# Optimization experiments

Measured on AMD Instinct MI355X. Metric: run time of the kernel, lower is better.

The kernel has to match this reference:

```python
import jax, jax.numpy as jnp
import numpy as np
from jax import lax

B, C, H, W = 8, 256, 128, 128
RED = 16


def _disk(r):
    yy, xx = np.mgrid[-r:r + 1, -r:r + 1]
    return ((xx * xx + yy * yy) <= r * r).astype(np.float32)


def _se_conv(m, se):
    kern = jnp.asarray(se)[None, None]  # [1,1,k,k]
    return lax.conv_general_dilated(m, kern, (1, 1), 'SAME',
                                    dimension_numbers=('NCHW', 'OIHW', 'NCHW'))


def _dilate(m, se):
    return (_se_conv(m, se) > 0.5).astype(m.dtype)


def _erode(m, se):
    return (_se_conv(m, se) > float(se.sum()) - 0.5).astype(m.dtype)


def _morph(mask):
    # GPU-friendly analogue of morphologic_process (skimage CPU round-trip):
    # invert, opening(disk2) ~ remove_small_objects(20), closing(disk1) ~
    # remove_small_holes(10), pad-3 binary_closing(disk3), crop, invert.
    d1, d2, d3 = _disk(1), _disk(2), _disk(3)
    m = 1.0 - mask
    m = _dilate(_erode(m, d2), d2)
    m = _erode(_dilate(m, d1), d1)
    mp = jnp.pad(m, ((0, 0), (0, 0), (3, 3), (3, 3)))
    mp = _erode(_dilate(mp, d3), d3)
    return 1.0 - mp[:, :, 3:-3, 3:-3]


def _conv1x1(x, w, b):
    return jnp.einsum('oi,bihw->bohw', w, x) + b[None, :, None, None]


def _avg3(x):
    # torch AvgPool2d(3,1,1) with count_include_pad=True -> always /9
    return lax.reduce_window(x, 0.0, lax.add, (1, 1, 3, 3), (1, 1, 1, 1), 'SAME') / 9.0


def _max3(x):
    return lax.reduce_window(x, -jnp.inf, lax.max, (1, 1, 3, 3), (1, 1, 1, 1), 'SAME')


def setup_inputs() -> dict:
    key = jax.random.key(0)
    ks = iter(jax.random.split(key, 32))
    s = 0.05
    d = {
        'x_p': jax.random.normal(next(ks), (B, C, H, W), jnp.float32),
        'x_c': jax.random.normal(next(ks), (B, C, H, W), jnp.float32),
        # PALayer: conv_p (shared two 1x1), conv_c (2c->c)
        'pa_w1': jax.random.normal(next(ks), (C, C), jnp.float32) * s,
        'pa_b1': jnp.zeros((C,), jnp.float32),
        'pa_w2': jax.random.normal(next(ks), (C, C), jnp.float32) * s,
        'pa_b2': jnp.zeros((C,), jnp.float32),
        'pa_wc': jax.random.normal(next(ks), (C, 2 * C), jnp.float32) * s,
        'pa_bc': jnp.zeros((C,), jnp.float32),
        # CALayer: conv_avg and conv_max (c -> c/16 -> c)
        'ca_aw1': jax.random.normal(next(ks), (C // RED, C), jnp.float32) * s,
        'ca_ab1': jnp.zeros((C // RED,), jnp.float32),
        'ca_aw2': jax.random.normal(next(ks), (C, C // RED), jnp.float32) * s,
        'ca_ab2': jnp.zeros((C,), jnp.float32),
        'ca_mw1': jax.random.normal(next(ks), (C // RED, C), jnp.float32) * s,
        'ca_mb1': jnp.zeros((C // RED,), jnp.float32),
        'ca_mw2': jax.random.normal(next(ks), (C, C // RED), jnp.float32) * s,
        'ca_mb2': jnp.zeros((C,), jnp.float32),
        # b1/b2/b3 1x1 convs
        'b1_w': jax.random.normal(next(ks), (C, C), jnp.float32) * s,
        'b1_b': jnp.zeros((C,), jnp.float32),
        'b2_w': jax.random.normal(next(ks), (C, C), jnp.float32) * s,
        'b2_b': jnp.zeros((C,), jnp.float32),
        'b3_w': jax.random.normal(next(ks), (C, C), jnp.float32) * s,
        'b3_b': jnp.zeros((C,), jnp.float32),
        # fusion: (2c+1) -> c
        'fus_w': jax.random.normal(next(ks), (C, 2 * C + 1), jnp.float32) * s,
        'fus_b': jnp.zeros((C,), jnp.float32),
    }
    return d


def reference(x_p, x_c, pa_w1, pa_b1, pa_w2, pa_b2, pa_wc, pa_bc,
              ca_aw1, ca_ab1, ca_aw2, ca_ab2, ca_mw1, ca_mb1, ca_mw2, ca_mb2,
              b1_w, b1_b, b2_w, b2_b, b3_w, b3_b, fus_w, fus_b):
    b, c, h, w = x_p.shape
    # --- PALayer(x_p) ---
    y1 = _avg3(x_p)
    y2 = _max3(x_p)
    y3 = _conv1x1(jax.nn.relu(_conv1x1(y1, pa_w1, pa_b1)), pa_w2, pa_b2)
    y4 = _conv1x1(jax.nn.relu(_conv1x1(y2, pa_w1, pa_b1)), pa_w2, pa_b2)
    pa_gate = jax.nn.sigmoid(_conv1x1(jnp.concatenate([y1 + y3, y2 + y4], axis=1), pa_wc, pa_bc))
    buffer_p = pa_gate * x_p
    # --- CALayer(x_c) ---
    a = jnp.mean(x_c, axis=(2, 3), keepdims=True)
    m = jnp.max(x_c, axis=(2, 3), keepdims=True)
    ya = _conv1x1(jax.nn.relu(_conv1x1(a, ca_aw1, ca_ab1)), ca_aw2, ca_ab2)
    ym = _conv1x1(jax.nn.relu(_conv1x1(m, ca_mw1, ca_mb1)), ca_mw2, ca_mb2)
    buffer_c = jax.nn.sigmoid(ya + ym) * x_c
    # --- cross-modal width attention ---
    Q1 = _conv1x1(buffer_p, b1_w, b1_b)
    S1 = _conv1x1(buffer_c, b2_w, b2_b)
    M_c_to_p = jax.nn.softmax(jnp.einsum('bchi,bchj->bhij', Q1, S1), axis=-1)
    Q2 = _conv1x1(buffer_c, b1_w, b1_b)
    S2 = _conv1x1(buffer_p, b2_w, b2_b)
    M_p_to_c = jax.nn.softmax(jnp.einsum('bchi,bchj->bhij', Q2, S2), axis=-1)
    # validity mask (detached) + morphology
    V = (jnp.sum(lax.stop_gradient(M_p_to_c), axis=2) > 0.1).astype(x_p.dtype)  # [b,h,w]
    V = _morph(V[:, None])  # [b,1,h,w]
    # attend b3(x_c) with M_c_to_p
    v3 = _conv1x1(x_c, b3_w, b3_b)
    buf = jnp.einsum('bhij,bchj->bchi', M_c_to_p, v3)
    out = _conv1x1(jnp.concatenate([buf, x_p, V], axis=1), fus_w, fus_b)
    return out
```

## Files before the change

### kernel.cpp

```cpp
#include <hip/hip_runtime.h>
#include <hip/hip_bf16.h>
#include <math.h>

#define BB 8
#define CC 256
#define HH 128
#define WW 128
#define HWSZ (HH*WW)
#define NTOT ((size_t)BB*CC*HWSZ)

typedef __hip_bfloat16 bf16;
typedef __attribute__((ext_vector_type(8))) short short8v;
typedef __attribute__((ext_vector_type(4))) float f32x4;

__device__ __forceinline__ float ldf(const float* p) { return *p; }
__device__ __forceinline__ float ldf(const bf16* p) { return __bfloat162float(*p); }
__device__ __forceinline__ void stf(float* p, float v) { *p = v; }
__device__ __forceinline__ void stf(bf16* p, float v) { *p = __float2bfloat16(v); }

union bfu { bf16 b; unsigned short u; };
__device__ __forceinline__ unsigned short f2bf_bits(float v) { bfu c; c.b = __float2bfloat16(v); return c.u; }
__device__ __forceinline__ float bfbits2f(unsigned short u) { bfu c; c.u = u; return __bfloat162float(c.b); }
__device__ __forceinline__ unsigned pk2(float a, float b) {
    return (unsigned)f2bf_bits(a) | ((unsigned)f2bf_bits(b) << 16);
}

__global__ __launch_bounds__(256) void pool3_kernel(const float* __restrict__ x,
                                                    bf16* __restrict__ yavg,
                                                    bf16* __restrict__ ymax) {
    size_t idx = (size_t)blockIdx.x * 256 + threadIdx.x;
    int w0 = (int)(idx & 15) * 8;
    int h = (int)(idx >> 4) & 127;
    size_t bc = idx >> 11;
    const float* base = x + bc * HWSZ;
    float ts[8], tm[8];
#pragma unroll
    for (int i = 0; i < 8; ++i) { ts[i] = 0.f; tm[i] = -INFINITY; }
#pragma unroll
    for (int dy = -1; dy <= 1; ++dy) {
        int hh = h + dy;
        if (hh < 0 || hh >= HH) continue;
        const float* rp = base + hh * WW + w0;
        float4 v0 = *(const float4*)rp;
        float4 v1 = *(const float4*)(rp + 4);
        float s9[10], m9[10];
        s9[1] = v0.x; s9[2] = v0.y; s9[3] = v0.z; s9[4] = v0.w;
        s9[5] = v1.x; s9[6] = v1.y; s9[7] = v1.z; s9[8] = v1.w;
#pragma unroll
        for (int i = 1; i < 9; ++i) m9[i] = s9[i];
        if (w0 > 0)      { float L = rp[-1]; s9[0] = L; m9[0] = L; }
        else             { s9[0] = 0.f; m9[0] = -INFINITY; }
        if (w0 < WW - 8) { float R = rp[8]; s9[9] = R; m9[9] = R; }
        else             { s9[9] = 0.f; m9[9] = -INFINITY; }
#pragma unroll
        for (int i = 0; i < 8; ++i) {
            ts[i] += s9[i] + s9[i + 1] + s9[i + 2];
            tm[i] = fmaxf(tm[i], fmaxf(m9[i], fmaxf(m9[i + 1], m9[i + 2])));
        }
    }
    uint4 ua, um;
    ua.x = pk2(ts[0] * (1.f/9.f), ts[1] * (1.f/9.f));
    ua.y = pk2(ts[2] * (1.f/9.f), ts[3] * (1.f/9.f));
    ua.z = pk2(ts[4] * (1.f/9.f), ts[5] * (1.f/9.f));
    ua.w = pk2(ts[6] * (1.f/9.f), ts[7] * (1.f/9.f));
    um.x = pk2(tm[0], tm[1]); um.y = pk2(tm[2], tm[3]);
    um.z = pk2(tm[4], tm[5]); um.w = pk2(tm[6], tm[7]);
    *(uint4*)(yavg + idx * 8) = ua;
    *(uint4*)(ymax + idx * 8) = um;
}

#define EPI_NONE   0
#define EPI_RELU   1
#define EPI_ADDAUX 2
#define EPI_SIGMUL 3

#define BMP 128
#define BNO 128
#define BKC 64
#define LDK 72

template<bool SC, class T>
__device__ __forceinline__ unsigned short ld_bits(const T* p, float s);
template<> __device__ __forceinline__ unsigned short ld_bits<false, bf16>(const bf16* p, float) {
    bfu c; c.b = *p; return c.u;
}
template<> __device__ __forceinline__ unsigned short ld_bits<true, bf16>(const bf16* p, float s) {
    return f2bf_bits(__bfloat162float(*p) * s);
}
template<> __device__ __forceinline__ unsigned short ld_bits<false, float>(const float* p, float) {
    return f2bf_bits(*p);
}
template<> __device__ __forceinline__ unsigned short ld_bits<true, float>(const float* p, float s) {
    return f2bf_bits(*p * s);
}

template<bool SC, class T>
__device__ __forceinline__ void stage_X(short* __restrict__ Xs,
                                        const T* __restrict__ in,
                                        const float* __restrict__ scale,
                                        int b, int cbase, size_t pbase, int tid)
{
    const int xp  = tid & 127;
    const int xkh = (tid >> 7) * 32;
    const T* src = in + ((size_t)b * 256 + cbase + xkh) * HWSZ + pbase + xp;
    short* dst = Xs + xp * LDK + xkh;
#pragma unroll
    for (int ch = 0; ch < 2; ++ch) {
        unsigned short us[16];
#pragma unroll
        for (int g = 0; g < 4; ++g) {
#pragma unroll
            for (int r = 0; r < 4; ++r) {
                int kloc = ch * 16 + g * 4 + r;
                float sc = SC ? scale[b * 256 + cbase + xkh + kloc] : 1.f;
                us[g * 4 + r] = ld_bits<SC, T>(src + (size_t)kloc * HWSZ, sc);
            }
        }
#pragma unroll
        for (int g = 0; g < 4; ++g) {
            uint2 wv;
            wv.x = (unsigned)us[g * 4 + 0] | ((unsigned)us[g * 4 + 1] << 16);
            wv.y = (unsigned)us[g * 4 + 2] | ((unsigned)us[g * 4 + 3] << 16);
            *(uint2*)(dst + g * 8 + ch * 4) = wv;
        }
    }
}

__device__ __forceinline__ void stage_W(short* __restrict__ Wh, short* __restrict__ Wl,
                                        const float* __restrict__ Wm, int WS,
                                        int obase, int k0, int tid)
{
    const int wo  = tid >> 1;
    const int wkh = (tid & 1) * 32;
    const float* wrow = Wm + (size_t)(obase + wo) * WS + k0 + wkh;
    short* dh = Wh + wo * LDK + wkh;
    short* dl = Wl + wo * LDK + wkh;
#pragma unroll
    for (int ch = 0; ch < 2; ++ch) {
        unsigned short uh[16], ul[16];
#pragma unroll
        for (int g = 0; g < 4; ++g) {
#pragma unroll
            for (int r = 0; r < 4; ++r) {
                float v = wrow[ch * 16 + g * 4 + r];
                unsigned short hb = f2bf_bits(v);
                uh[g * 4 + r] = hb;
                ul[g * 4 + r] = f2bf_bits(v - bfbits2f(hb));
            }
        }
#pragma unroll
        for (int g = 0; g < 4; ++g) {
            uint2 a, c;
            a.x = (unsigned)uh[g*4+0] | ((unsigned)uh[g*4+1] << 16);
            a.y = (unsigned)uh[g*4+2] | ((unsigned)uh[g*4+3] << 16);
            c.x = (unsigned)ul[g*4+0] | ((unsigned)ul[g*4+1] << 16);
            c.y = (unsigned)ul[g*4+2] | ((unsigned)ul[g*4+3] << 16);
            *(uint2*)(dh + g * 8 + ch * 4) = a;
            *(uint2*)(dl + g * 8 + ch * 4) = c;
        }
    }
}

__device__ __forceinline__ void stage_rm(short* __restrict__ Xs, const bf16* __restrict__ src,
                                         size_t rstride, int k0, int tid)
{
    const int row = tid & 127;
    const int kh = (tid >> 7) * 32;
    const short* sp = (const short*)src + (size_t)row * rstride + k0 + kh;
    short* dst = Xs + row * LDK + kh;
#pragma unroll
    for (int q = 0; q < 4; ++q) {
        short8v v = *(const short8v*)(sp + q * 8);
        uint2 lo, hi;
        lo.x = (unsigned)(unsigned short)v[0] | ((unsigned)(unsigned short)v[1] << 16);
        lo.y = (unsigned)(unsigned short)v[2] | ((unsigned)(unsigned short)v[3] << 16);
        hi.x = (unsigned)(unsigned short)v[4] | ((unsigned)(unsigned short)v[5] << 16);
        hi.y = (unsigned)(unsigned short)v[6] | ((unsigned)(unsigned short)v[7] << 16);
        *(uint2*)(dst + ((2*q) & 3) * 8 + (q >> 1) * 4) = lo;
        *(uint2*)(dst + ((2*q+1) & 3) * 8 + (q >> 1) * 4) = hi;
    }
}

__device__ __forceinline__ void load4f(const bf16* p, float* v) {
    ushort4 u = *(const ushort4*)p;
    v[0] = bfbits2f(u.x); v[1] = bfbits2f(u.y); v[2] = bfbits2f(u.z); v[3] = bfbits2f(u.w);
}
__device__ __forceinline__ void load4f(const float* p, float* v) {
    float4 u = *(const float4*)p;
    v[0] = u.x; v[1] = u.y; v[2] = u.z; v[3] = u.w;
}
__device__ __forceinline__ void store4(bf16* p, const float* v) {
    uint2 u;
    u.x = pk2(v[0], v[1]);
    u.y = pk2(v[2], v[3]);
    *(uint2*)p = u;
}
__device__ __forceinline__ void store4(float* p, const float* v) {
    *(float4*)p = make_float4(v[0], v[1], v[2], v[3]);
}

template<int MODE, bool TWO_IN, bool HAS_SCALE, bool HAS_V,
         class TIN1, class TIN2, class TAUX, class TOUT>
__global__ __launch_bounds__(256) void conv1x1_kernel(
    TOUT* __restrict__ out,
    const TIN1* __restrict__ in1,
    const TIN2* __restrict__ in2,
    const float* __restrict__ Wm, int WS,
    const float* __restrict__ bias,
    const TAUX* __restrict__ aux,
    const float* __restrict__ scale,
    const float* __restrict__ vvec,
    const float* __restrict__ vw)
{
    const int K = TWO_IN ? 512 : 256;
    __shared__ __align__(16) short Xs[BMP * LDK];
    __shared__ __align__(16) short Wh[BNO * LDK];
    __shared__ __align__(16) short Wl[BNO * LDK];
    const int tid = threadIdx.x;
    const int b = blockIdx.z;
    const size_t p0 = (size_t)blockIdx.x * BMP;
    const int o0 = blockIdx.y * BNO;
    const int lane = tid & 63, wave = tid >> 6;
    const int wr = wave >> 1, wc = wave & 1;
    const int lrow = lane & 15, lg = lane >> 4;

    f32x4 acc[4][4];
#pragma unroll
    for (int mi = 0; mi < 4; ++mi)
#pragma unroll
        for (int ni = 0; ni < 4; ++ni) acc[mi][ni] = (f32x4)(0.f);

    for (int kt = 0; kt < K / BKC; ++kt) {
        const int k0 = kt * BKC;
        stage_W(Wh, Wl, Wm, WS, o0, k0, tid);
        if (TWO_IN && k0 >= 256)
            stage_X<false, TIN2>(Xs, in2, nullptr, b, k0 - 256, p0, tid);
        else
            stage_X<HAS_SCALE, TIN1>(Xs, in1, scale, b, k0, p0, tid);
        __syncthreads();
#pragma unroll
        for (int kk = 0; kk < 2; ++kk) {
            short8v af[4], bh[4], bl[4];
#pragma unroll
            for (int mi = 0; mi < 4; ++mi)
                af[mi] = *(const short8v*)&Xs[(wr * 64 + mi * 16 + lrow) * LDK + kk * 32 + lg * 8];
#pragma unroll
            for (int ni = 0; ni < 4; ++ni) {
                bh[ni] = *(const short8v*)&Wh[(wc * 64 + ni * 16 + lrow) * LDK + kk * 32 + lg * 8];
                bl[ni] = *(const short8v*)&Wl[(wc * 64 + ni * 16 + lrow) * LDK + kk * 32 + lg * 8];
            }
#pragma unroll
            for (int mi = 0; mi < 4; ++mi)
#pragma unroll
                for (int ni = 0; ni < 4; ++ni)
                    acc[mi][ni] = __builtin_amdgcn_mfma_f32_16x16x32_bf16(af[mi], bh[ni], acc[mi][ni], 0, 0, 0);
#pragma unroll
            for (int mi = 0; mi < 4; ++mi)
#pragma unroll
                for (int ni = 0; ni < 4; ++ni)
                    acc[mi][ni] = __builtin_amdgcn_mfma_f32_16x16x32_bf16(af[mi], bl[ni], acc[mi][ni], 0, 0, 0);
        }
        __syncthreads();
    }

#pragma unroll
    for (int ni = 0; ni < 4; ++ni) {
        const int o = o0 + wc * 64 + ni * 16 + lrow;
        const float bs = bias[o];
        const float vwo = HAS_V ? vw[(size_t)o * WS] : 0.f;
#pragma unroll
        for (int mi = 0; mi < 4; ++mi) {
            const size_t p = p0 + wr * 64 + mi * 16 + lg * 4;
            const size_t oidx = ((size_t)b * CC + o) * HWSZ + p;
            float auxv[4];
            if (MODE == EPI_ADDAUX || MODE == EPI_SIGMUL) load4f(&aux[oidx], auxv);
            float vv[4];
            if (HAS_V) load4f(&vvec[(size_t)b * HWSZ + p], vv);
            float vals[4];
#pragma unroll
            for (int r = 0; r < 4; ++r) {
                float val = acc[mi][ni][r] + bs;
                if (HAS_V) val += vwo * vv[r];
                if (MODE == EPI_RELU)        val = fmaxf(val, 0.f);
                else if (MODE == EPI_ADDAUX) val += auxv[r];
                else if (MODE == EPI_SIGMUL) val = (1.f / (1.f + __expf(-val))) * auxv[r];
                vals[r] = val;
            }
            store4(&out[oidx], vals);
        }
    }
}

__global__ __launch_bounds__(256) void ca_reduce_kernel(const float* __restrict__ xc,
                                                        float* __restrict__ avgv,
                                                        float* __restrict__ maxv) {
    int bc = blockIdx.x;
    const float4* base = (const float4*)(xc + (size_t)bc * HWSZ);
    float s = 0.f, mx = -INFINITY;
    for (int i = threadIdx.x; i < HWSZ / 4; i += 256) {
        float4 v = base[i];
        s += v.x + v.y + v.z + v.w;
        mx = fmaxf(mx, fmaxf(fmaxf(v.x, v.y), fmaxf(v.z, v.w)));
    }
    for (int off = 32; off; off >>= 1) {
        s += __shfl_down(s, off);
        mx = fmaxf(mx, __shfl_down(mx, off));
    }
    __shared__ float ss[4], sm[4];
    int wid = threadIdx.x >> 6, lane = threadIdx.x & 63;
    if (lane == 0) { ss[wid] = s; sm[wid] = mx; }
    __syncthreads();
    if (threadIdx.x == 0) {
        float S = ss[0] + ss[1] + ss[2] + ss[3];
        float M = fmaxf(fmaxf(sm[0], sm[1]), fmaxf(sm[2], sm[3]));
        avgv[bc] = S * (1.f / HWSZ);
        maxv[bc] = M;
    }
}

__global__ __launch_bounds__(256) void ca_mlp_kernel(
    const float* __restrict__ avgv, const float* __restrict__ maxv,
    const float* __restrict__ aw1, const float* __restrict__ ab1,
    const float* __restrict__ aw2, const float* __restrict__ ab2,
    const float* __restrict__ mw1, const float* __restrict__ mb1,
    const float* __restrict__ mw2, const float* __restrict__ mb2,
    float* __restrict__ gate) {
    int b = blockIdx.x;
    __shared__ float av[256], mv[256], ha[16], hm[16];
    int t = threadIdx.x;
    av[t] = avgv[b * 256 + t];
    mv[t] = maxv[b * 256 + t];
    __syncthreads();
    if (t < 16) {
        float s = ab1[t];
        for (int i = 0; i < 256; ++i) s += aw1[t * 256 + i] * av[i];
        ha[t] = fmaxf(s, 0.f);
    } else if (t < 32) {
        int r = t - 16;
        float s = mb1[r];
        for (int i = 0; i < 256; ++i) s += mw1[r * 256 + i] * mv[i];
        hm[r] = fmaxf(s, 0.f);
    }
    __syncthreads();
    float ya = ab2[t], ym = mb2[t];
    for (int r = 0; r < 16; ++r) {
        ya += aw2[t * 16 + r] * ha[r];
        ym += mw2[t * 16 + r] * hm[r];
    }
    float g = ya + ym;
    gate[b * 256 + t] = 1.f / (1.f + __expf(-g));
}

template<bool STORE_M>
__global__ __launch_bounds__(256) void attn_kernel(
    const bf16* __restrict__ Q, const bf16* __restrict__ S,
    bf16* __restrict__ Mout, float* __restrict__ m0out)
{
    int bh = blockIdx.x; int b = bh >> 7, h = bh & 127;
    const bf16* Qb = Q + (size_t)b * CC * HWSZ + h * WW;
    const bf16* Sb = S + (size_t)b * CC * HWSZ + h * WW;
    __shared__ __align__(16) short Qs[128 * LDK];
    __shared__ __align__(16) short Ss[128 * LDK];
    const int tid = threadIdx.x;
    const int lane = tid & 63, wave = tid >> 6;
    const int lrow = lane & 15, lg = lane >> 4;

    f32x4 acc[2][8];
#pragma unroll
    for (int mi = 0; mi < 2; ++mi)
#pragma unroll
        for (int ni = 0; ni < 8; ++ni) acc[mi][ni] = (f32x4)(0.f);

    for (int kt = 0; kt < 4; ++kt) {
        const int k0 = kt * 64;
        {
            const int xp = tid & 127, xkh = (tid >> 7) * 32;
            const bf16* sq = Qb + (size_t)(k0 + xkh) * HWSZ + xp;
            const bf16* ssrc = Sb + (size_t)(k0 + xkh) * HWSZ + xp;
            short* dq = Qs + xp * LDK + xkh;
            short* ds = Ss + xp * LDK + xkh;
#pragma unroll
            for (int ch = 0; ch < 2; ++ch) {
#pragma unroll
                for (int g = 0; g < 4; ++g) {
                    unsigned short uq[4], us[4];
#pragma unroll
                    for (int r = 0; r < 4; ++r) {
                        int kloc = ch * 16 + g * 4 + r;
                        bfu cq; cq.b = sq[(size_t)kloc * HWSZ]; uq[r] = cq.u;
                        bfu cs2; cs2.b = ssrc[(size_t)kloc * HWSZ]; us[r] = cs2.u;
                    }
                    uint2 wq, ws;
                    wq.x = (unsigned)uq[0] | ((unsigned)uq[1] << 16);
                    wq.y = (unsigned)uq[2] | ((unsigned)uq[3] << 16);
                    ws.x = (unsigned)us[0] | ((unsigned)us[1] << 16);
                    ws.y = (unsigned)us[2] | ((unsigned)us[3] << 16);
                    *(uint2*)(dq + g * 8 + ch * 4) = wq;
                    *(uint2*)(ds + g * 8 + ch * 4) = ws;
                }
            }
        }
        __syncthreads();
#pragma unroll
        for (int kk = 0; kk < 2; ++kk) {
            short8v qa[2], sv[8];
#pragma unroll
            for (int mi = 0; mi < 2; ++mi)
                qa[mi] = *(const short8v*)&Qs[(wave * 32 + mi * 16 + lrow) * LDK + kk * 32 + lg * 8];
#pragma unroll
            for (int ni = 0; ni < 8; ++ni)
                sv[ni] = *(const short8v*)&Ss[(ni * 16 + lrow) * LDK + kk * 32 + lg * 8];
#pragma unroll
            for (int mi = 0; mi < 2; ++mi)
#pragma unroll
                for (int ni = 0; ni < 8; ++ni)
                    acc[mi][ni] = __builtin_amdgcn_mfma_f32_16x16x32_bf16(qa[mi], sv[ni], acc[mi][ni], 0, 0, 0);
        }
        __syncthreads();
    }

#pragma unroll
    for (int mi = 0; mi < 2; ++mi) {
#pragma unroll
        for (int r = 0; r < 4; ++r) {
            float mx = acc[mi][0][r];
#pragma unroll
            for (int ni = 1; ni < 8; ++ni) mx = fmaxf(mx, acc[mi][ni][r]);
            for (int m = 1; m < 16; m <<= 1) mx = fmaxf(mx, __shfl_xor(mx, m));
            float sm = 0.f;
#pragma unroll
            for (int ni = 0; ni < 8; ++ni) {
                float e = __expf(acc[mi][ni][r] - mx);
                acc[mi][ni][r] = e; sm += e;
            }
            for (int m = 1; m < 16; m <<= 1) sm += __shfl_xor(sm, m);
            float inv = 1.f / sm;
#pragma unroll
            for (int ni = 0; ni < 8; ++ni) acc[mi][ni][r] *= inv;
        }
    }

    if (STORE_M) {
        bf16* Mb = Mout + (size_t)bh * WW * WW;
#pragma unroll
        for (int mi = 0; mi < 2; ++mi)
#pragma unroll
            for (int r = 0; r < 4; ++r) {
                int i = wave * 32 + mi * 16 + lg * 4 + r;
#pragma unroll
                for (int ni = 0; ni < 8; ++ni)
                    stf(&Mb[i * WW + ni * 16 + lrow], acc[mi][ni][r]);
            }
    } else {
        __shared__ float cs[16][128];
#pragma unroll
        for (int ni = 0; ni < 8; ++ni) {
            float s = 0.f;
#pragma unroll
            for (int mi = 0; mi < 2; ++mi)
#pragma unroll
                for (int r = 0; r < 4; ++r) s += acc[mi][ni][r];
            cs[wave * 4 + lg][ni * 16 + lrow] = s;
        }
        __syncthreads();
        if (tid < 128) {
            float s = 0.f;
#pragma unroll
            for (int g = 0; g < 16; ++g) s += cs[g][tid];
            m0out[(size_t)b * HWSZ + h * WW + tid] = (s > 0.1f) ? 0.f : 1.f;
        }
    }
}

__global__ __launch_bounds__(256) void attn_apply_kernel(
    const bf16* __restrict__ Mbuf, const bf16* __restrict__ v3,
    bf16* __restrict__ outb)
{
    int bh = blockIdx.x; int b = bh >> 7, h = bh & 127;
    int ch0 = blockIdx.y * 128;
    const bf16* Mb = Mbuf + (size_t)bh * WW * WW;
    const bf16* Vb = v3 + ((size_t)b * CC + ch0) * HWSZ + h * WW;
    bf16* Ob = outb + ((size_t)b * CC + ch0) * HWSZ + h * WW;
    __shared__ __align__(16) short Ms[128 * LDK];
    __shared__ __align__(16) short Vs[128 * LDK];
    const int tid = threadIdx.x;
    const int lane = tid & 63, wave = tid >> 6;
    const int lrow = lane & 15, lg = lane >> 4;

    f32x4 acc[2][8];
#pragma unroll
    for (int mi = 0; mi < 2; ++mi)
#pragma unroll
        for (int ni = 0; ni < 8; ++ni) acc[mi][ni] = (f32x4)(0.f);

    for (int kt = 0; kt < 2; ++kt) {
        const int k0 = kt * 64;
        stage_rm(Ms, Mb, WW, k0, tid);
        stage_rm(Vs, Vb, HWSZ, k0, tid);
        __syncthreads();
#pragma unroll
        for (int kk = 0; kk < 2; ++kk) {
            short8v ma[2], vv[8];
#pragma unroll
            for (int mi = 0; mi < 2; ++mi)
                ma[mi] = *(const short8v*)&Ms[(wave * 32 + mi * 16 + lrow) * LDK + kk * 32 + lg * 8];
#pragma unroll
            for (int ni = 0; ni < 8; ++ni)
                vv[ni] = *(const short8v*)&Vs[(ni * 16 + lrow) * LDK + kk * 32 + lg * 8];
#pragma unroll
            for (int mi = 0; mi < 2; ++mi)
#pragma unroll
                for (int ni = 0; ni < 8; ++ni)
                    acc[mi][ni] = __builtin_amdgcn_mfma_f32_16x16x32_bf16(ma[mi], vv[ni], acc[mi][ni], 0, 0, 0);
        }
        __syncthreads();
    }

#pragma unroll
    for (int ni = 0; ni < 8; ++ni) {
        const int c = ni * 16 + lrow;
#pragma unroll
        for (int mi = 0; mi < 2; ++mi) {
            const int i0 = wave * 32 + mi * 16 + lg * 4;
            float vals[4] = { acc[mi][ni][0], acc[mi][ni][1], acc[mi][ni][2], acc[mi][ni][3] };
            store4(&Ob[(size_t)c * HWSZ + i0], vals);
        }
    }
}

__global__ void morph_kernel(const float* __restrict__ in, float* __restrict__ out,
                             int Hd, int Wd, int r, float thresh) {
    int idx = blockIdx.x * 256 + threadIdx.x;
    int tot = BB * Hd * Wd;
    if (idx >= tot) return;
    int x = idx % Wd; int y = (idx / Wd) % Hd; int b = idx / (Wd * Hd);
    const float* base = in + (size_t)b * Hd * Wd;
    float s = 0.f;
    for (int dy = -r; dy <= r; ++dy) {
        int yy = y + dy; if (yy < 0 || yy >= Hd) continue;
        for (int dx = -r; dx <= r; ++dx) {
            if (dx * dx + dy * dy > r * r) continue;
            int xx = x + dx; if (xx < 0 || xx >= Wd) continue;
            s += base[yy * Wd + xx];
        }
    }
    out[idx] = (s > thresh) ? 1.f : 0.f;
}

__global__ void pad3_kernel(const float* __restrict__ in, float* __restrict__ out) {
    int idx = blockIdx.x * 256 + threadIdx.x;
    int tot = BB * 134 * 134; if (idx >= tot) return;
    int x = idx % 134; int y = (idx / 134) % 134; int b = idx / (134 * 134);
    float v = 0.f;
    int xs = x - 3, ys = y - 3;
    if (xs >= 0 && xs < 128 && ys >= 0 && ys < 128)
        v = in[((size_t)b * 128 + ys) * 128 + xs];
    out[idx] = v;
}

__global__ void vfinal_kernel(const float* __restrict__ in, float* __restrict__ V) {
    int idx = blockIdx.x * 256 + threadIdx.x;
    if (idx >= BB * HWSZ) return;
    int x = idx & 127; int y = (idx >> 7) & 127; int b = idx >> 14;
    V[idx] = 1.f - in[((size_t)b * 134 + y + 3) * 134 + (x + 3)];
}

extern "C" void kernel_launch(void* const* d_in, const int* in_sizes, int n_in,
                              void* d_out, int out_size, void* d_ws, size_t ws_size,
                              hipStream_t stream) {
    const float* x_p   = (const float*)d_in[0];
    const float* x_c   = (const float*)d_in[1];
    const float* pa_w1 = (const float*)d_in[2];
    const float* pa_b1 = (const float*)d_in[3];
    const float* pa_w2 = (const float*)d_in[4];
    const float* pa_b2 = (const float*)d_in[5];
    const float* pa_wc = (const float*)d_in[6];
    const float* pa_bc = (const float*)d_in[7];
    const float* ca_aw1 = (const float*)d_in[8];
    const float* ca_ab1 = (const float*)d_in[9];
    const float* ca_aw2 = (const float*)d_in[10];
    const float* ca_ab2 = (const float*)d_in[11];
    const float* ca_mw1 = (const float*)d_in[12];
    const float* ca_mb1 = (const float*)d_in[13];
    const float* ca_mw2 = (const float*)d_in[14];
    const float* ca_mb2 = (const float*)d_in[15];
    const float* b1_w  = (const float*)d_in[16];
    const float* b1_b  = (const float*)d_in[17];
    const float* b2_w  = (const float*)d_in[18];
    const float* b2_b  = (const float*)d_in[19];
    const float* b3_w  = (const float*)d_in[20];
    const float* b3_b  = (const float*)d_in[21];
    const float* fus_w = (const float*)d_in[22];
    const float* fus_b = (const float*)d_in[23];
    float* out = (float*)d_out;

    char* wsb = (char*)d_ws;
    bf16* A  = (bf16*)wsb;
    bf16* Bb = (bf16*)(wsb + NTOT * 2);
    float* smalls = (float*)(wsb + NTOT * 4);
    float* avgv = smalls;
    float* maxv = smalls + 2048;
    float* gate = smalls + 4096;
    float* mph0 = smalls + 6144;
    float* mph1 = mph0 + 143648;
    float* Vfin = mph1 + 143648;
    bf16* D1 = (bf16*)d_out;
    bf16* D2 = D1 + NTOT;
    bf16* Mbuf = D1;

    dim3 cgrid(HWSZ / BMP, CC / BNO, BB);
    const int TPB = 256;

    pool3_kernel<<<NTOT / 8 / 256, TPB, 0, stream>>>(x_p, A, Bb);
    conv1x1_kernel<EPI_RELU, false, false, false, bf16, bf16, bf16, bf16>
        <<<cgrid, TPB, 0, stream>>>(D1, A, nullptr, pa_w1, 256, pa_b1,
                                    nullptr, nullptr, nullptr, nullptr);
    conv1x1_kernel<EPI_ADDAUX, false, false, false, bf16, bf16, bf16, bf16>
        <<<cgrid, TPB, 0, stream>>>(D2, D1, nullptr, pa_w2, 256, pa_b2,
                                    A, nullptr, nullptr, nullptr);
    conv1x1_kernel<EPI_RELU, false, false, false, bf16, bf16, bf16, bf16>
        <<<cgrid, TPB, 0, stream>>>(A, Bb, nullptr, pa_w1, 256, pa_b1,
                                    nullptr, nullptr, nullptr, nullptr);
    conv1x1_kernel<EPI_ADDAUX, false, false, false, bf16, bf16, bf16, bf16>
        <<<cgrid, TPB, 0, stream>>>(D1, A, nullptr, pa_w2, 256, pa_b2,
                                    Bb, nullptr, nullptr, nullptr);
    conv1x1_kernel<EPI_SIGMUL, true, false, false, bf16, bf16, float, bf16>
        <<<cgrid, TPB, 0, stream>>>(A, D2, D1, pa_wc, 512, pa_bc,
                                    x_p, nullptr, nullptr, nullptr);

    ca_reduce_kernel<<<BB * CC, TPB, 0, stream>>>(x_c, avgv, maxv);
    ca_mlp_kernel<<<BB, TPB, 0, stream>>>(avgv, maxv, ca_aw1, ca_ab1, ca_aw2, ca_ab2,
                                          ca_mw1, ca_mb1, ca_mw2, ca_mb2, gate);

    conv1x1_kernel<EPI_NONE, false, false, false, bf16, bf16, bf16, bf16>
        <<<cgrid, TPB, 0, stream>>>(Bb, A, nullptr, b1_w, 256, b1_b,
                                    nullptr, nullptr, nullptr, nullptr);
    conv1x1_kernel<EPI_NONE, false, false, false, bf16, bf16, bf16, bf16>
        <<<cgrid, TPB, 0, stream>>>(D1, A, nullptr, b2_w, 256, b2_b,
                                    nullptr, nullptr, nullptr, nullptr);
    conv1x1_kernel<EPI_NONE, false, true, false, float, float, float, bf16>
        <<<cgrid, TPB, 0, stream>>>(A, x_c, nullptr, b1_w, 256, b1_b,
                                    nullptr, gate, nullptr, nullptr);
    conv1x1_kernel<EPI_NONE, false, true, false, float, float, float, bf16>
        <<<cgrid, TPB, 0, stream>>>(D2, x_c, nullptr, b2_w, 256, b2_b,
                                    nullptr, gate, nullptr, nullptr);

    attn_kernel<false><<<BB * HH, TPB, 0, stream>>>(A, D1, nullptr, mph0);
    attn_kernel<true><<<BB * HH, TPB, 0, stream>>>(Bb, D2, Mbuf, nullptr);

    conv1x1_kernel<EPI_NONE, false, false, false, float, float, float, bf16>
        <<<cgrid, TPB, 0, stream>>>(A, x_c, nullptr, b3_w, 256, b3_b,
                                    nullptr, nullptr, nullptr, nullptr);

    morph_kernel<<<512, TPB, 0, stream>>>(mph0, mph1, 128, 128, 2, 12.5f);
    morph_kernel<<<512, TPB, 0, stream>>>(mph1, mph0, 128, 128, 2, 0.5f);
    morph_kernel<<<512, TPB, 0, stream>>>(mph0, mph1, 128, 128, 1, 0.5f);
    morph_kernel<<<512, TPB, 0, stream>>>(mph1, mph0, 128, 128, 1, 4.5f);
    pad3_kernel<<<562, TPB, 0, stream>>>(mph0, mph1);
    morph_kernel<<<562, TPB, 0, stream>>>(mph1, mph0, 134, 134, 3, 0.5f);
    morph_kernel<<<562, TPB, 0, stream>>>(mph0, mph1, 134, 134, 3, 28.5f);
    vfinal_kernel<<<512, TPB, 0, stream>>>(mph1, Vfin);

    attn_apply_kernel<<<dim3(BB * HH, 2), TPB, 0, stream>>>(Mbuf, A, Bb);
    conv1x1_kernel<EPI_NONE, true, false, true, bf16, float, float, float>
        <<<cgrid, TPB, 0, stream>>>(out, Bb, x_p, fus_w, 513, fus_b,
                                    nullptr, nullptr, Vfin, fus_w + 512);
}
```

Baseline: 1.563 ms.

## Pre-split weights into swizzled bf16 tiles and load via global_load_lds

```diff
diff --git a/kernel.cpp b/kernel.cpp
--- a/kernel.cpp
+++ b/kernel.cpp
@@ -23,6 +23,12 @@
 __device__ __forceinline__ float bfbits2f(unsigned short u) { bfu c; c.u = u; return __bfloat162float(c.b); }
 __device__ __forceinline__ unsigned pk2(float a, float b) {
     return (unsigned)f2bf_bits(a) | ((unsigned)f2bf_bits(b) << 16);
+}
+
+__device__ __forceinline__ void gld16(const void* g, void* l) {
+    __builtin_amdgcn_global_load_lds(
+        (const __attribute__((address_space(1))) unsigned int*)(uintptr_t)g,
+        (__attribute__((address_space(3))) unsigned int*)(uintptr_t)l, 16, 0, 0);
 }
 
 __global__ __launch_bounds__(256) void pool3_kernel(const float* __restrict__ x,
@@ -69,6 +75,33 @@
     *(uint4*)(ymax + idx * 8) = um;
 }
 
+__global__ __launch_bounds__(256) void prep_w_kernel(
+    const float* __restrict__ w0, const float* __restrict__ w1,
+    const float* __restrict__ w2, const float* __restrict__ w3,
+    const float* __restrict__ w4, const float* __restrict__ w5,
+    const float* __restrict__ w6, short* __restrict__ dst)
+{
+    int gid = blockIdx.x * 256 + threadIdx.x;
+    const float* src; int K, WS, local; size_t dofs;
+    if (gid < 65536)       { src = w0; K = 256; WS = 256; dofs = 0;      local = gid; }
+    else if (gid < 131072) { src = w1; K = 256; WS = 256; dofs = 131072; local = gid - 65536; }
+    else if (gid < 262144) { src = w2; K = 512; WS = 512; dofs = 262144; local = gid - 131072; }
+    else if (gid < 327680) { src = w3; K = 256; WS = 256; dofs = 524288; local = gid - 262144; }
+    else if (gid < 393216) { src = w4; K = 256; WS = 256; dofs = 655360; local = gid - 327680; }
+    else if (gid < 458752) { src = w5; K = 256; WS = 256; dofs = 786432; local = gid - 393216; }
+    else                   { src = w6; K = 512; WS = 513; dofs = 917504; local = gid - 458752; }
+    int o = (K == 256) ? (local >> 8) : (local >> 9);
+    int k = local & (K - 1);
+    int kt = k >> 6, k6 = k & 63, k5 = k6 & 31;
+    int pos = (k6 >> 5) * 32 + ((k5 >> 2) & 3) * 8 + (k5 >> 4) * 4 + (k5 & 3);
+    pos ^= (o & 7) << 3;
+    size_t off = dofs + (size_t)(o >> 7) * K * 128 + (size_t)kt * 8192 + (size_t)(o & 127) * 64 + pos;
+    float v = src[(size_t)o * WS + k];
+    unsigned short hb = f2bf_bits(v);
+    dst[off] = (short)hb;
+    dst[off + (size_t)256 * K] = (short)f2bf_bits(v - bfbits2f(hb));
+}
+
 #define EPI_NONE   0
 #define EPI_RELU   1
 #define EPI_ADDAUX 2
@@ -76,8 +109,6 @@
 
 #define BMP 128
 #define BNO 128
-#define BKC 64
-#define LDK 72
 
 template<bool SC, class T>
 __device__ __forceinline__ unsigned short ld_bits(const T* p, float s);
@@ -103,61 +134,23 @@
     const int xp  = tid & 127;
     const int xkh = (tid >> 7) * 32;
     const T* src = in + ((size_t)b * 256 + cbase + xkh) * HWSZ + pbase + xp;
-    short* dst = Xs + xp * LDK + xkh;
-#pragma unroll
-    for (int ch = 0; ch < 2; ++ch) {
-        unsigned short us[16];
-#pragma unroll
-        for (int g = 0; g < 4; ++g) {
-#pragma unroll
-            for (int r = 0; r < 4; ++r) {
-                int kloc = ch * 16 + g * 4 + r;
-                float sc = SC ? scale[b * 256 + cbase + xkh + kloc] : 1.f;
-                us[g * 4 + r] = ld_bits<SC, T>(src + (size_t)kloc * HWSZ, sc);
-            }
-        }
-#pragma unroll
-        for (int g = 0; g < 4; ++g) {
-            uint2 wv;
-            wv.x = (unsigned)us[g * 4 + 0] | ((unsigned)us[g * 4 + 1] << 16);
-            wv.y = (unsigned)us[g * 4 + 2] | ((unsigned)us[g * 4 + 3] << 16);
-            *(uint2*)(dst + g * 8 + ch * 4) = wv;
-        }
-    }
-}
-
-__device__ __forceinline__ void stage_W(short* __restrict__ Wh, short* __restrict__ Wl,
-                                        const float* __restrict__ Wm, int WS,
-                                        int obase, int k0, int tid)
-{
-    const int wo  = tid >> 1;
-    const int wkh = (tid & 1) * 32;
-    const float* wrow = Wm + (size_t)(obase + wo) * WS + k0 + wkh;
-    short* dh = Wh + wo * LDK + wkh;
-    short* dl = Wl + wo * LDK + wkh;
-#pragma unroll
-    for (int ch = 0; ch < 2; ++ch) {
-        unsigned short uh[16], ul[16];
-#pragma unroll
-        for (int g = 0; g < 4; ++g) {
-#pragma unroll
-            for (int r = 0; r < 4; ++r) {
-                float v = wrow[ch * 16 + g * 4 + r];
-                unsigned short hb = f2bf_bits(v);
-                uh[g * 4 + r] = hb;
-                ul[g * 4 + r] = f2bf_bits(v - bfbits2f(hb));
-            }
-        }
-#pragma unroll
-        for (int g = 0; g < 4; ++g) {
-            uint2 a, c;
-            a.x = (unsigned)uh[g*4+0] | ((unsigned)uh[g*4+1] << 16);
-            a.y = (unsigned)uh[g*4+2] | ((unsigned)uh[g*4+3] << 16);
-            c.x = (unsigned)ul[g*4+0] | ((unsigned)ul[g*4+1] << 16);
-            c.y = (unsigned)ul[g*4+2] | ((unsigned)ul[g*4+3] << 16);
-            *(uint2*)(dh + g * 8 + ch * 4) = a;
-            *(uint2*)(dl + g * 8 + ch * 4) = c;
-        }
+    const float* scp = SC ? (scale + b * 256 + cbase + xkh) : nullptr;
+    const int swz = (xp & 7) << 3;
+    short* dst = Xs + xp * 64;
+#pragma unroll
+    for (int g = 0; g < 4; ++g) {
+        unsigned short u[8];
+#pragma unroll
+        for (int j = 0; j < 8; ++j) {
+            int k5 = (j >> 2) * 16 + g * 4 + (j & 3);
+            u[j] = ld_bits<SC, T>(src + (size_t)k5 * HWSZ, SC ? scp[k5] : 1.f);
+        }
+        uint4 wv;
+        wv.x = (unsigned)u[0] | ((unsigned)u[1] << 16);
+        wv.y = (unsigned)u[2] | ((unsigned)u[3] << 16);
+        wv.z = (unsigned)u[4] | ((unsigned)u[5] << 16);
+        wv.w = (unsigned)u[6] | ((unsigned)u[7] << 16);
+        *(uint4*)(dst + ((xkh + g * 8) ^ swz)) = wv;
     }
 }
 
@@ -167,17 +160,25 @@
     const int row = tid & 127;
     const int kh = (tid >> 7) * 32;
     const short* sp = (const short*)src + (size_t)row * rstride + k0 + kh;
-    short* dst = Xs + row * LDK + kh;
-#pragma unroll
-    for (int q = 0; q < 4; ++q) {
-        short8v v = *(const short8v*)(sp + q * 8);
-        uint2 lo, hi;
-        lo.x = (unsigned)(unsigned short)v[0] | ((unsigned)(unsigned short)v[1] << 16);
-        lo.y = (unsigned)(unsigned short)v[2] | ((unsigned)(unsigned short)v[3] << 16);
-        hi.x = (unsigned)(unsigned short)v[4] | ((unsigned)(unsigned short)v[5] << 16);
-        hi.y = (unsigned)(unsigned short)v[6] | ((unsigned)(unsigned short)v[7] << 16);
-        *(uint2*)(dst + ((2*q) & 3) * 8 + (q >> 1) * 4) = lo;
-        *(uint2*)(dst + ((2*q+1) & 3) * 8 + (q >> 1) * 4) = hi;
+    const int swz = (row & 7) << 3;
+    short* dst = Xs + row * 64;
+    short8v lv[4];
+#pragma unroll
+    for (int q = 0; q < 4; ++q) lv[q] = *(const short8v*)(sp + q * 8);
+#pragma unroll
+    for (int g = 0; g < 4; ++g) {
+        unsigned short u[8];
+#pragma unroll
+        for (int r = 0; r < 4; ++r) {
+            u[r]     = (unsigned short)lv[g >> 1][(g & 1) * 4 + r];
+            u[4 + r] = (unsigned short)lv[2 + (g >> 1)][(g & 1) * 4 + r];
+        }
+        uint4 wv;
+        wv.x = (unsigned)u[0] | ((unsigned)u[1] << 16);
+        wv.y = (unsigned)u[2] | ((unsigned)u[3] << 16);
+        wv.z = (unsigned)u[4] | ((unsigned)u[5] << 16);
+        wv.w = (unsigned)u[6] | ((unsigned)u[7] << 16);
+        *(uint4*)(dst + ((kh + g * 8) ^ swz)) = wv;
     }
 }
 
@@ -205,24 +206,26 @@
     TOUT* __restrict__ out,
     const TIN1* __restrict__ in1,
     const TIN2* __restrict__ in2,
-    const float* __restrict__ Wm, int WS,
+    const short* __restrict__ Wp,
     const float* __restrict__ bias,
     const TAUX* __restrict__ aux,
     const float* __restrict__ scale,
     const float* __restrict__ vvec,
-    const float* __restrict__ vw)
+    const float* __restrict__ vw, int vws)
 {
     const int K = TWO_IN ? 512 : 256;
-    __shared__ __align__(16) short Xs[BMP * LDK];
-    __shared__ __align__(16) short Wh[BNO * LDK];
-    __shared__ __align__(16) short Wl[BNO * LDK];
+    __shared__ __align__(16) short Xs[BMP * 64];
+    __shared__ __align__(16) short Wh[BNO * 64];
+    __shared__ __align__(16) short Wl[BNO * 64];
     const int tid = threadIdx.x;
     const int b = blockIdx.z;
     const size_t p0 = (size_t)blockIdx.x * BMP;
     const int o0 = blockIdx.y * BNO;
-    const int lane = tid & 63, wave = tid >> 6;
+    const int lane = tid & 63;
+    const int wave = tid >> 6;
     const int wr = wave >> 1, wc = wave & 1;
     const int lrow = lane & 15, lg = lane >> 4;
+    const int sA = (lrow & 7) << 3;
 
     f32x4 acc[4][4];
 #pragma unroll
@@ -230,9 +233,19 @@
 #pragma unroll
         for (int ni = 0; ni < 4; ++ni) acc[mi][ni] = (f32x4)(0.f);
 
-    for (int kt = 0; kt < K / BKC; ++kt) {
-        const int k0 = kt * BKC;
-        stage_W(Wh, Wl, Wm, WS, o0, k0, tid);
+    for (int kt = 0; kt < K / 64; ++kt) {
+        const int k0 = kt * 64;
+        {
+            const short* gWh = Wp + (size_t)(o0 >> 7) * K * 128 + (size_t)kt * 8192;
+            const short* gWl = gWh + (size_t)256 * K;
+            const int wofs = wave * 4096;
+            const int lb = lane * 16;
+#pragma unroll
+            for (int q = 0; q < 4; ++q) {
+                gld16((const char*)gWh + wofs + q * 1024 + lb, (char*)Wh + wofs + q * 1024);
+                gld16((const char*)gWl + wofs + q * 1024 + lb, (char*)Wl + wofs + q * 1024);
+            }
+        }
         if (TWO_IN && k0 >= 256)
             stage_X<false, TIN2>(Xs, in2, nullptr, b, k0 - 256, p0, tid);
         else
@@ -240,14 +253,15 @@
         __syncthreads();
 #pragma unroll
         for (int kk = 0; kk < 2; ++kk) {
+            const int kofs = kk * 32 + lg * 8;
             short8v af[4], bh[4], bl[4];
 #pragma unroll
             for (int mi = 0; mi < 4; ++mi)
-                af[mi] = *(const short8v*)&Xs[(wr * 64 + mi * 16 + lrow) * LDK + kk * 32 + lg * 8];
+                af[mi] = *(const short8v*)&Xs[(wr * 64 + mi * 16 + lrow) * 64 + (kofs ^ sA)];
 #pragma unroll
             for (int ni = 0; ni < 4; ++ni) {
-                bh[ni] = *(const short8v*)&Wh[(wc * 64 + ni * 16 + lrow) * LDK + kk * 32 + lg * 8];
-                bl[ni] = *(const short8v*)&Wl[(wc * 64 + ni * 16 + lrow) * LDK + kk * 32 + lg * 8];
+                bh[ni] = *(const short8v*)&Wh[(wc * 64 + ni * 16 + lrow) * 64 + (kofs ^ sA)];
+                bl[ni] = *(const short8v*)&Wl[(wc * 64 + ni * 16 + lrow) * 64 + (kofs ^ sA)];
             }
 #pragma unroll
             for (int mi = 0; mi < 4; ++mi)
@@ -267,7 +281,7 @@
     for (int ni = 0; ni < 4; ++ni) {
         const int o = o0 + wc * 64 + ni * 16 + lrow;
         const float bs = bias[o];
-        const float vwo = HAS_V ? vw[(size_t)o * WS] : 0.f;
+        const float vwo = HAS_V ? vw[(size_t)o * vws] : 0.f;
 #pragma unroll
         for (int mi = 0; mi < 4; ++mi) {
             const size_t p = p0 + wr * 64 + mi * 16 + lg * 4;
@@ -359,11 +373,12 @@
     int bh = blockIdx.x; int b = bh >> 7, h = bh & 127;
     const bf16* Qb = Q + (size_t)b * CC * HWSZ + h * WW;
     const bf16* Sb = S + (size_t)b * CC * HWSZ + h * WW;
-    __shared__ __align__(16) short Qs[128 * LDK];
-    __shared__ __align__(16) short Ss[128 * LDK];
+    __shared__ __align__(16) short Qs[128 * 64];
+    __shared__ __align__(16) short Ss[128 * 64];
     const int tid = threadIdx.x;
     const int lane = tid & 63, wave = tid >> 6;
     const int lrow = lane & 15, lg = lane >> 4;
+    const int sA = (lrow & 7) << 3;
 
     f32x4 acc[2][8];
 #pragma unroll
@@ -377,39 +392,42 @@
             const int xp = tid & 127, xkh = (tid >> 7) * 32;
             const bf16* sq = Qb + (size_t)(k0 + xkh) * HWSZ + xp;
             const bf16* ssrc = Sb + (size_t)(k0 + xkh) * HWSZ + xp;
-            short* dq = Qs + xp * LDK + xkh;
-            short* ds = Ss + xp * LDK + xkh;
-#pragma unroll
-            for (int ch = 0; ch < 2; ++ch) {
-#pragma unroll
-                for (int g = 0; g < 4; ++g) {
-                    unsigned short uq[4], us[4];
-#pragma unroll
-                    for (int r = 0; r < 4; ++r) {
-                        int kloc = ch * 16 + g * 4 + r;
-                        bfu cq; cq.b = sq[(size_t)kloc * HWSZ]; uq[r] = cq.u;
-                        bfu cs2; cs2.b = ssrc[(size_t)kloc * HWSZ]; us[r] = cs2.u;
-                    }
-                    uint2 wq, ws;
-                    wq.x = (unsigned)uq[0] | ((unsigned)uq[1] << 16);
-                    wq.y = (unsigned)uq[2] | ((unsigned)uq[3] << 16);
-                    ws.x = (unsigned)us[0] | ((unsigned)us[1] << 16);
-                    ws.y = (unsigned)us[2] | ((unsigned)us[3] << 16);
-                    *(uint2*)(dq + g * 8 + ch * 4) = wq;
-                    *(uint2*)(ds + g * 8 + ch * 4) = ws;
+            const int swz = (xp & 7) << 3;
+            short* dq = Qs + xp * 64;
+            short* dsx = Ss + xp * 64;
+#pragma unroll
+            for (int g = 0; g < 4; ++g) {
+                unsigned short uq[8], us[8];
+#pragma unroll
+                for (int j = 0; j < 8; ++j) {
+                    int k5 = (j >> 2) * 16 + g * 4 + (j & 3);
+                    bfu cq; cq.b = sq[(size_t)k5 * HWSZ]; uq[j] = cq.u;
+                    bfu cs2; cs2.b = ssrc[(size_t)k5 * HWSZ]; us[j] = cs2.u;
                 }
+                uint4 a, s2;
+                a.x = (unsigned)uq[0] | ((unsigned)uq[1] << 16);
+                a.y = (unsigned)uq[2] | ((unsigned)uq[3] << 16);
+                a.z = (unsigned)uq[4] | ((unsigned)uq[5] << 16);
+                a.w = (unsigned)uq[6] | ((unsigned)uq[7] << 16);
+                s2.x = (unsigned)us[0] | ((unsigned)us[1] << 16);
+                s2.y = (unsigned)us[2] | ((unsigned)us[3] << 16);
+                s2.z = (unsigned)us[4] | ((unsigned)us[5] << 16);
+                s2.w = (unsigned)us[6] | ((unsigned)us[7] << 16);
+                *(uint4*)(dq + ((xkh + g * 8) ^ swz)) = a;
+                *(uint4*)(dsx + ((xkh + g * 8) ^ swz)) = s2;
             }
         }
         __syncthreads();
 #pragma unroll
         for (int kk = 0; kk < 2; ++kk) {
+            const int kofs = (kk * 32 + lg * 8) ^ sA;
             short8v qa[2], sv[8];
 #pragma unroll
             for (int mi = 0; mi < 2; ++mi)
-                qa[mi] = *(const short8v*)&Qs[(wave * 32 + mi * 16 + lrow) * LDK + kk * 32 + lg * 8];
+                qa[mi] = *(const short8v*)&Qs[(wave * 32 + mi * 16 + lrow) * 64 + kofs];
 #pragma unroll
             for (int ni = 0; ni < 8; ++ni)
-                sv[ni] = *(const short8v*)&Ss[(ni * 16 + lrow) * LDK + kk * 32 + lg * 8];
+                sv[ni] = *(const short8v*)&Ss[(ni * 16 + lrow) * 64 + kofs];
 #pragma unroll
             for (int mi = 0; mi < 2; ++mi)
 #pragma unroll
@@ -481,11 +499,12 @@
     const bf16* Mb = Mbuf + (size_t)bh * WW * WW;
     const bf16* Vb = v3 + ((size_t)b * CC + ch0) * HWSZ + h * WW;
     bf16* Ob = outb + ((size_t)b * CC + ch0) * HWSZ + h * WW;
-    __shared__ __align__(16) short Ms[128 * LDK];
-    __shared__ __align__(16) short Vs[128 * LDK];
+    __shared__ __align__(16) short Ms[128 * 64];
+    __shared__ __align__(16) short Vs[128 * 64];
     const int tid = threadIdx.x;
     const int lane = tid & 63, wave = tid >> 6;
     const int lrow = lane & 15, lg = lane >> 4;
+    const int sA = (lrow & 7) << 3;
 
     f32x4 acc[2][8];
 #pragma unroll
@@ -500,13 +519,14 @@
         __syncthreads();
 #pragma unroll
         for (int kk = 0; kk < 2; ++kk) {
+            const int kofs = (kk * 32 + lg * 8) ^ sA;
             short8v ma[2], vv[8];
 #pragma unroll
             for (int mi = 0; mi < 2; ++mi)
-                ma[mi] = *(const short8v*)&Ms[(wave * 32 + mi * 16 + lrow) * LDK + kk * 32 + lg * 8];
+                ma[mi] = *(const short8v*)&Ms[(wave * 32 + mi * 16 + lrow) * 64 + kofs];
 #pragma unroll
             for (int ni = 0; ni < 8; ++ni)
-                vv[ni] = *(const short8v*)&Vs[(ni * 16 + lrow) * LDK + kk * 32 + lg * 8];
+                vv[ni] = *(const short8v*)&Vs[(ni * 16 + lrow) * 64 + kofs];
 #pragma unroll
             for (int mi = 0; mi < 2; ++mi)
 #pragma unroll
@@ -604,6 +624,14 @@
     float* mph0 = smalls + 6144;
     float* mph1 = mph0 + 143648;
     float* Vfin = mph1 + 143648;
+    short* Wprep = (short*)(wsb + NTOT * 4 + 1703936);
+    const short* Wp_paw1 = Wprep + 0;
+    const short* Wp_paw2 = Wprep + 131072;
+    const short* Wp_pawc = Wprep + 262144;
+    const short* Wp_b1   = Wprep + 524288;
+    const short* Wp_b2   = Wprep + 655360;
+    const short* Wp_b3   = Wprep + 786432;
+    const short* Wp_fus  = Wprep + 917504;
     bf16* D1 = (bf16*)d_out;
     bf16* D2 = D1 + NTOT;
     bf16* Mbuf = D1;
@@ -611,46 +639,48 @@
     dim3 cgrid(HWSZ / BMP, CC / BNO, BB);
     const int TPB = 256;
 
+    prep_w_kernel<<<2304, TPB, 0, stream>>>(pa_w1, pa_w2, pa_wc, b1_w, b2_w, b3_w, fus_w, Wprep);
+
     pool3_kernel<<<NTOT / 8 / 256, TPB, 0, stream>>>(x_p, A, Bb);
     conv1x1_kernel<EPI_RELU, false, false, false, bf16, bf16, bf16, bf16>
-        <<<cgrid, TPB, 0, stream>>>(D1, A, nullptr, pa_w1, 256, pa_b1,
-                                    nullptr, nullptr, nullptr, nullptr);
+        <<<cgrid, TPB, 0, stream>>>(D1, A, nullptr, Wp_paw1, pa_b1,
+                                    nullptr, nullptr, nullptr, nullptr, 0);
     conv1x1_kernel<EPI_ADDAUX, false, false, false, bf16, bf16, bf16, bf16>
-        <<<cgrid, TPB, 0, stream>>>(D2, D1, nullptr, pa_w2, 256, pa_b2,
-                                    A, nullptr, nullptr, nullptr);
+        <<<cgrid, TPB, 0, stream>>>(D2, D1, nullptr, Wp_paw2, pa_b2,
+                                    A, nullptr, nullptr, nullptr, 0);
     conv1x1_kernel<EPI_RELU, false, false, false, bf16, bf16, bf16, bf16>
-        <<<cgrid, TPB, 0, stream>>>(A, Bb, nullptr, pa_w1, 256, pa_b1,
-                                    nullptr, nullptr, nullptr, nullptr);
+        <<<cgrid, TPB, 0, stream>>>(A, Bb, nullptr, Wp_paw1, pa_b1,
+                                    nullptr, nullptr, nullptr, nullptr, 0);
     conv1x1_kernel<EPI_ADDAUX, false, false, false, bf16, bf16, bf16, bf16>
-        <<<cgrid, TPB, 0, stream>>>(D1, A, nullptr, pa_w2, 256, pa_b2,
-                                    Bb, nullptr, nullptr, nullptr);
+        <<<cgrid, TPB, 0, stream>>>(D1, A, nullptr, Wp_paw2, pa_b2,
+                                    Bb, nullptr, nullptr, nullptr, 0);
     conv1x1_kernel<EPI_SIGMUL, true, false, false, bf16, bf16, float, bf16>
-        <<<cgrid, TPB, 0, stream>>>(A, D2, D1, pa_wc, 512, pa_bc,
-                                    x_p, nullptr, nullptr, nullptr);
+        <<<cgrid, TPB, 0, stream>>>(A, D2, D1, Wp_pawc, pa_bc,
+                                    x_p, nullptr, nullptr, nullptr, 0);
 
     ca_reduce_kernel<<<BB * CC, TPB, 0, stream>>>(x_c, avgv, maxv);
     ca_mlp_kernel<<<BB, TPB, 0, stream>>>(avgv, maxv, ca_aw1, ca_ab1, ca_aw2, ca_ab2,
                                           ca_mw1, ca_mb1, ca_mw2, ca_mb2, gate);
 
     conv1x1_kernel<EPI_NONE, false, false, false, bf16, bf16, bf16, bf16>
-        <<<cgrid, TPB, 0, stream>>>(Bb, A, nullptr, b1_w, 256, b1_b,
-                                    nullptr, nullptr, nullptr, nullptr);
+        <<<cgrid, TPB, 0, stream>>>(Bb, A, nullptr, Wp_b1, b1_b,
+                                    nullptr, nullptr, nullptr, nullptr, 0);
     conv1x1_kernel<EPI_NONE, false, false, false, bf16, bf16, bf16, bf16>
-        <<<cgrid, TPB, 0, stream>>>(D1, A, nullptr, b2_w, 256, b2_b,
-                                    nullptr, nullptr, nullptr, nullptr);
+        <<<cgrid, TPB, 0, stream>>>(D1, A, nullptr, Wp_b2, b2_b,
+                                    nullptr, nullptr, nullptr, nullptr, 0);
     conv1x1_kernel<EPI_NONE, false, true, false, float, float, float, bf16>
-        <<<cgrid, TPB, 0, stream>>>(A, x_c, nullptr, b1_w, 256, b1_b,
-                                    nullptr, gate, nullptr, nullptr);
+        <<<cgrid, TPB, 0, stream>>>(A, x_c, nullptr, Wp_b1, b1_b,
+                                    nullptr, gate, nullptr, nullptr, 0);
     conv1x1_kernel<EPI_NONE, false, true, false, float, float, float, bf16>
-        <<<cgrid, TPB, 0, stream>>>(D2, x_c, nullptr, b2_w, 256, b2_b,
-                                    nullptr, gate, nullptr, nullptr);
+        <<<cgrid, TPB, 0, stream>>>(D2, x_c, nullptr, Wp_b2, b2_b,
+                                    nullptr, gate, nullptr, nullptr, 0);
 
     attn_kernel<false><<<BB * HH, TPB, 0, stream>>>(A, D1, nullptr, mph0);
     attn_kernel<true><<<BB * HH, TPB, 0, stream>>>(Bb, D2, Mbuf, nullptr);
 
     conv1x1_kernel<EPI_NONE, false, false, false, float, float, float, bf16>
-        <<<cgrid, TPB, 0, stream>>>(A, x_c, nullptr, b3_w, 256, b3_b,
-                                    nullptr, nullptr, nullptr, nullptr);
+        <<<cgrid, TPB, 0, stream>>>(A, x_c, nullptr, Wp_b3, b3_b,
+                                    nullptr, nullptr, nullptr, nullptr, 0);
 
     morph_kernel<<<512, TPB, 0, stream>>>(mph0, mph1, 128, 128, 2, 12.5f);
     morph_kernel<<<512, TPB, 0, stream>>>(mph1, mph0, 128, 128, 2, 0.5f);
@@ -663,6 +693,6 @@
 
     attn_apply_kernel<<<dim3(BB * HH, 2), TPB, 0, stream>>>(Mbuf, A, Bb);
     conv1x1_kernel<EPI_NONE, true, false, true, bf16, float, float, float>
-        <<<cgrid, TPB, 0, stream>>>(out, Bb, x_p, fus_w, 513, fus_b,
-                                    nullptr, nullptr, Vfin, fus_w + 512);
-}
+        <<<cgrid, TPB, 0, stream>>>(out, Bb, x_p, Wp_fus, fus_b,
+                                    nullptr, nullptr, Vfin, fus_w + 512, 513);
+}
```

After: 1.414 ms. 1.11x faster.
